# Kernel tuning notes

Measured on AMD Instinct MI355X. Metric: run time of the kernel, lower is better.

Reference implementation:

```python
import jax, jax.numpy as jnp
import numpy as np

N = 10000
E = 160000
C = 256        # in_channels
M = 256        # mid_channels
R = 64         # nregion


def _glorot(key, shape):
    fan_in, fan_out = shape[-1], shape[0]
    lim = (6.0 / (fan_in + fan_out)) ** 0.5
    return jax.random.uniform(key, shape, jnp.float32, -lim, lim)


def setup_inputs() -> dict:
    key = jax.random.key(0)
    ks = jax.random.split(key, 12)
    x = jax.random.normal(ks[0], (N, C), jnp.float32)
    edge_index = jax.random.randint(ks[1], (2, E), 0, N, jnp.int32)
    conv_w = _glorot(ks[2], (C, C))
    conv_b = jnp.zeros((C,), jnp.float32)
    lin1_w = _glorot(ks[3], (M, C)); lin1_b = jnp.zeros((M,), jnp.float32)
    lin2_w = _glorot(ks[4], (M, M)); lin2_b = jnp.zeros((M,), jnp.float32)
    lin3_w = _glorot(ks[5], (1, M)); lin3_b = jnp.zeros((1,), jnp.float32)
    lin4_w = _glorot(ks[6], (M, M)); lin4_b = jnp.zeros((M,), jnp.float32)
    bilin_w = _glorot(ks[7], (R, M, M)) * 0.1
    bilin_b = jnp.zeros((R,), jnp.float32)
    return {"x": x, "edge_index": edge_index,
            "conv_w": conv_w, "conv_b": conv_b,
            "lin1_w": lin1_w, "lin1_b": lin1_b,
            "lin2_w": lin2_w, "lin2_b": lin2_b,
            "lin3_w": lin3_w, "lin3_b": lin3_b,
            "lin4_w": lin4_w, "lin4_b": lin4_b,
            "bilin_w": bilin_w, "bilin_b": bilin_b}


def gcn_conv(x, edge_index, w, b):
    # PyG GCNConv: add self-loops, symmetric D^-1/2 (A+I) D^-1/2 normalization
    src, dst = edge_index[0], edge_index[1]
    n = x.shape[0]
    xw = x @ w.T                                            # [N, C]
    deg = jnp.ones((n,), xw.dtype).at[dst].add(jnp.ones((E,), xw.dtype))  # +1 for self loop
    dinv = jax.lax.rsqrt(deg)
    norm = dinv[src] * dinv[dst]                            # [E]
    agg = jnp.zeros_like(xw).at[dst].add(norm[:, None] * xw[src])
    agg = agg + (dinv * dinv)[:, None] * xw                 # self-loop messages
    return agg + b


def reference(x, edge_index, conv_w, conv_b, lin1_w, lin1_b, lin2_w, lin2_b,
              lin3_w, lin3_b, lin4_w, lin4_b, bilin_w, bilin_b):
    out = jax.nn.relu(gcn_conv(x, edge_index, conv_w, conv_b))
    x0 = out + x                                            # residual [N, C]
    x0 = jax.nn.relu(x0 @ lin1_w.T + lin1_b)                # [N, M]
    x1 = jax.nn.relu(x0 @ lin2_w.T + lin2_b)
    x1 = x1 @ lin3_w.T + lin3_b                             # [N, 1]
    x2 = jax.nn.relu(x0 @ lin4_w.T + lin4_b)                # [N, M]
    # Bilinear(x2, x2): out[n,r] = x2[n] @ W[r] @ x2[n] + b[r]
    t = (x2 @ bilin_w.reshape(R * M, M).T).reshape(-1, R, M)  # [N, R, M]
    x2 = jnp.sum(t * x2[:, None, :], axis=-1) + bilin_b       # [N, R]
    return (x1, x2)
```

## Files before the change

kernel.cpp:

```cpp
#include <hip/hip_runtime.h>

typedef unsigned short u16;
typedef __attribute__((ext_vector_type(8))) short bf16x8;
typedef __attribute__((ext_vector_type(8))) unsigned short u16x8;
typedef __attribute__((ext_vector_type(4))) float f32x4;

#define N_NODES 10000
#define E_EDGES 160000
#define CX_N 2560000
#define W_N  65536
#define WB_N 4194304
#define CANON_BIG_BLOCKS 3426
#define HIST_BLOCKS 79

__device__ __forceinline__ float b2f(u16 u) {
  union { unsigned i; float f; } c; c.i = ((unsigned)u) << 16; return c.f;
}
__device__ __forceinline__ u16 f2b(float f) {
  union { float f; unsigned i; } c; c.f = f;
  unsigned i = c.i;
  return (u16)((i + 0x7FFFu + ((i >> 16) & 1u)) >> 16);
}

__global__ void detect_kernel(const unsigned* __restrict__ w, int* __restrict__ flag) {
  int t = threadIdx.x;
  int cnt = 0;
  for (int i = t; i < 1024; i += 64) {
    unsigned e = (w[i] >> 7) & 0xFF;
    cnt += (e >= 100 && e <= 145) ? 1 : 0;
  }
  for (int o = 32; o; o >>= 1) cnt += __shfl_xor(cnt, o);
  if (t == 0) *flag = (cnt >= 512) ? 1 : 0;
}

__global__ void canon_all_kernel(const void* sx, const void* swc, const void* sw1,
                                 const void* sw2, const void* sw4, const void* swB,
                                 const void* sbc, const void* sb1, const void* sb2,
                                 const void* sb4, const void* sw3, const void* sbB,
                                 const void* sb3,
                                 u16* __restrict__ dstBase,
                                 u16* cbc, u16* cb1, u16* cb2, u16* cb4,
                                 u16* cw3, u16* cbB, u16* cb3,
                                 const int* __restrict__ ei, int* __restrict__ count,
                                 const int* __restrict__ flag) {
  int b = blockIdx.x;
  int f = *flag;
  if (b < CANON_BIG_BLOCKS) {
    long e = ((long)b * 256 + threadIdx.x) * 8;
    const void* src; long so;
    if (e < CX_N)                { src = sx;  so = e; }
    else if (e < CX_N + W_N)     { src = swc; so = e - CX_N; }
    else if (e < CX_N + 2 * W_N) { src = sw1; so = e - (CX_N + W_N); }
    else if (e < CX_N + 3 * W_N) { src = sw2; so = e - (CX_N + 2 * W_N); }
    else if (e < CX_N + 4 * W_N) { src = sw4; so = e - (CX_N + 3 * W_N); }
    else                         { src = swB; so = e - (CX_N + 4 * W_N); }
    if (f) {
      u16x8 v = *((const u16x8*)((const u16*)src + so));
      *(u16x8*)(dstBase + e) = v;
    } else {
      const float* fp = (const float*)src + so;
      float4 a = *(const float4*)fp;
      float4 c = *(const float4*)(fp + 4);
      u16x8 o;
      o[0] = f2b(a.x); o[1] = f2b(a.y); o[2] = f2b(a.z); o[3] = f2b(a.w);
      o[4] = f2b(c.x); o[5] = f2b(c.y); o[6] = f2b(c.z); o[7] = f2b(c.w);
      *(u16x8*)(dstBase + e) = o;
    }
  } else if (b == CANON_BIG_BLOCKS) {
    int t = threadIdx.x;
    const void* srcs[7] = {sbc, sb1, sb2, sb4, sw3, sbB, sb3};
    u16* dsts[7] = {cbc, cb1, cb2, cb4, cw3, cbB, cb3};
    const int ns[7] = {256, 256, 256, 256, 256, 64, 1};
#pragma unroll
    for (int k = 0; k < 7; ++k) {
      if (t < ns[k]) {
        if (f) dsts[k][t] = ((const u16*)srcs[k])[t];
        else   dsts[k][t] = f2b(((const float*)srcs[k])[t]);
      }
    }
  } else {
    int base = (b - CANON_BIG_BLOCKS - 1) * 2048 + threadIdx.x * 8;
#pragma unroll
    for (int k = 0; k < 8; ++k) {
      int i = base + k;
      if (i < E_EDGES) atomicAdd(&count[ei[E_EDGES + i]], 1);
    }
  }
}

__device__ __forceinline__ void stage_async(const u16* __restrict__ src, int stride,
                                            int row0, int maxRow, int k0,
                                            u16* lds, int w, int lane) {
  int rsel = lane >> 3;
  int gch = (lane & 7) ^ rsel;
#pragma unroll
  for (int i = 0; i < 4; ++i) {
    int rb = (w * 4 + i) * 8;
    int grow = row0 + rb + rsel;
    grow = grow > maxRow ? maxRow : grow;
    const u16* gp = src + (size_t)grow * stride + k0 + gch * 8;
    u16* lp = lds + rb * 64;
    __builtin_amdgcn_global_load_lds(
        (const __attribute__((address_space(1))) void*)gp,
        (__attribute__((address_space(3))) void*)lp, 16, 0, 0);
  }
}

__device__ __forceinline__ void mma_tile(const u16* lA, const u16* lB,
                                         f32x4 acc[4][4], int wr, int wc, int lane) {
#pragma unroll
  for (int ks = 0; ks < 2; ++ks) {
    bf16x8 af[4], bfr[4];
    int g = ks * 4 + (lane >> 4);
#pragma unroll
    for (int t = 0; t < 4; ++t) {
      int rowA = wr * 64 + t * 16 + (lane & 15);
      af[t] = *(const bf16x8*)(lA + rowA * 64 + ((g ^ (rowA & 7)) * 8));
      int rowB = wc * 64 + t * 16 + (lane & 15);
      bfr[t] = *(const bf16x8*)(lB + rowB * 64 + ((g ^ (rowB & 7)) * 8));
    }
#pragma unroll
    for (int ti = 0; ti < 4; ++ti)
#pragma unroll
      for (int tj = 0; tj < 4; ++tj)
        acc[ti][tj] = __builtin_amdgcn_mfma_f32_16x16x32_bf16(af[ti], bfr[tj],
                                                              acc[ti][tj], 0, 0, 0);
  }
}

template <bool RELU, bool F32OUT>
__global__ __launch_bounds__(256, 2)
void gemm_kernel(const u16* __restrict__ A, const u16* __restrict__ B,
                 const u16* __restrict__ bias, float* __restrict__ outF,
                 u16* __restrict__ outB, int NN, int J, int K) {
  __shared__ u16 lA[128 * 64];
  __shared__ u16 lB[128 * 64];
  int lane = threadIdx.x & 63;
  int w = threadIdx.x >> 6;
  int wr = w >> 1, wc = w & 1;
  int n0 = blockIdx.y * 128;
  int j0 = blockIdx.x * 128;
  f32x4 acc[4][4];
#pragma unroll
  for (int i = 0; i < 4; ++i)
#pragma unroll
    for (int j = 0; j < 4; ++j) acc[i][j] = (f32x4){0.f, 0.f, 0.f, 0.f};

  for (int kt = 0; kt < K; kt += 64) {
    stage_async(A, K, n0, NN - 1, kt, lA, w, lane);
    stage_async(B, K, j0, J - 1, kt, lB, w, lane);
    __syncthreads();
    mma_tile(lA, lB, acc, wr, wc, lane);
    __syncthreads();
  }

#pragma unroll
  for (int ti = 0; ti < 4; ++ti)
#pragma unroll
    for (int tj = 0; tj < 4; ++tj) {
      int col = j0 + wc * 64 + tj * 16 + (lane & 15);
      float bv = bias ? b2f(bias[col]) : 0.0f;
#pragma unroll
      for (int r = 0; r < 4; ++r) {
        int row = n0 + wr * 64 + ti * 16 + ((lane >> 4) << 2) + r;
        if (row < NN) {
          float v = acc[ti][tj][r] + bv;
          if (RELU) v = fmaxf(v, 0.0f);
          if (F32OUT) outF[(size_t)row * J + col] = v;
          else        outB[(size_t)row * J + col] = f2b(v);
        }
      }
    }
}

__global__ __launch_bounds__(256, 2)
void gemm_fused234_kernel(const u16* __restrict__ A, const u16* __restrict__ B,
                          const u16* __restrict__ bias, const u16* __restrict__ w3,
                          float* __restrict__ out1acc, u16* __restrict__ x2v, int NN) {
  __shared__ u16 lA[128 * 64];
  __shared__ u16 lB[128 * 64];
  int lane = threadIdx.x & 63;
  int w = threadIdx.x >> 6;
  int wr = w >> 1, wc = w & 1;
  int n0 = blockIdx.y * 128;
  int j0 = blockIdx.x * 128;
  f32x4 acc[4][4];
#pragma unroll
  for (int i = 0; i < 4; ++i)
#pragma unroll
    for (int j = 0; j < 4; ++j) acc[i][j] = (f32x4){0.f, 0.f, 0.f, 0.f};

  for (int kt = 0; kt < 256; kt += 64) {
    stage_async(A, 256, n0, NN - 1, kt, lA, w, lane);
    stage_async(B, 256, j0, 511, kt, lB, w, lane);
    __syncthreads();
    mma_tile(lA, lB, acc, wr, wc, lane);
    __syncthreads();
  }

  if (j0 < 256) {
    float part[4][4];
#pragma unroll
    for (int ti = 0; ti < 4; ++ti)
#pragma unroll
      for (int r = 0; r < 4; ++r) part[ti][r] = 0.0f;
#pragma unroll
    for (int ti = 0; ti < 4; ++ti)
#pragma unroll
      for (int tj = 0; tj < 4; ++tj) {
        int col = j0 + wc * 64 + tj * 16 + (lane & 15);
        float bv = b2f(bias[col]);
        float wv = b2f(w3[col]);
#pragma unroll
        for (int r = 0; r < 4; ++r) {
          float v = fmaxf(acc[ti][tj][r] + bv, 0.0f);
          part[ti][r] += v * wv;
        }
      }
#pragma unroll
    for (int ti = 0; ti < 4; ++ti)
#pragma unroll
      for (int r = 0; r < 4; ++r) {
        float s = part[ti][r];
        s += __shfl_xor(s, 1);
        s += __shfl_xor(s, 2);
        s += __shfl_xor(s, 4);
        s += __shfl_xor(s, 8);
        if ((lane & 15) == 0) {
          int row = n0 + wr * 64 + ti * 16 + ((lane >> 4) << 2) + r;
          if (row < NN) unsafeAtomicAdd(&out1acc[row], s);
        }
      }
  } else {
#pragma unroll
    for (int ti = 0; ti < 4; ++ti)
#pragma unroll
      for (int tj = 0; tj < 4; ++tj) {
        int col = j0 + wc * 64 + tj * 16 + (lane & 15);
        float bv = b2f(bias[col]);
#pragma unroll
        for (int r = 0; r < 4; ++r) {
          int row = n0 + wr * 64 + ti * 16 + ((lane >> 4) << 2) + r;
          if (row < NN) {
            float v = fmaxf(acc[ti][tj][r] + bv, 0.0f);
            x2v[(size_t)row * 256 + (col - 256)] = f2b(v);
          }
        }
      }
  }
}

__global__ __launch_bounds__(256, 2)
void bilinear_kernel(const u16* __restrict__ x2v, const u16* __restrict__ W,
                     float* __restrict__ out2acc, int NN) {
  __shared__ u16 lA[128 * 64];
  __shared__ u16 lB[128 * 64];
  int lane = threadIdx.x & 63;
  int w = threadIdx.x >> 6;
  int wr = w >> 1, wc = w & 1;
  int n0 = blockIdx.y * 128;
  int rm0 = blockIdx.x * 128;
  int m0g = rm0 & 255;
  int xv_kt = (m0g >> 6) + wc;
  f32x4 acc[4][4];
#pragma unroll
  for (int i = 0; i < 4; ++i)
#pragma unroll
    for (int j = 0; j < 4; ++j) acc[i][j] = (f32x4){0.f, 0.f, 0.f, 0.f};

  u16 xvr[4][16];

#pragma unroll
  for (int kt4 = 0; kt4 < 4; ++kt4) {
    stage_async(x2v, 256, n0, NN - 1, kt4 * 64, lA, w, lane);
    stage_async(W, 256, rm0, 16383, kt4 * 64, lB, w, lane);
    __syncthreads();
    mma_tile(lA, lB, acc, wr, wc, lane);
    if (kt4 == xv_kt) {
#pragma unroll
      for (int tj = 0; tj < 4; ++tj) {
        int kl = tj * 16 + (lane & 15);
        int ch = kl >> 3, off = kl & 7;
#pragma unroll
        for (int ti = 0; ti < 4; ++ti)
#pragma unroll
          for (int r = 0; r < 4; ++r) {
            int rowl = wr * 64 + ti * 16 + ((lane >> 4) << 2) + r;
            xvr[tj][ti * 4 + r] = lA[rowl * 64 + ((ch ^ (rowl & 7)) * 8) + off];
          }
      }
    }
    __syncthreads();
  }

  int region = rm0 >> 8;
  float rowsum[4][4];
#pragma unroll
  for (int ti = 0; ti < 4; ++ti)
#pragma unroll
    for (int r = 0; r < 4; ++r) rowsum[ti][r] = 0.0f;

#pragma unroll
  for (int ti = 0; ti < 4; ++ti)
#pragma unroll
    for (int tj = 0; tj < 4; ++tj)
#pragma unroll
      for (int r = 0; r < 4; ++r)
        rowsum[ti][r] += acc[ti][tj][r] * b2f(xvr[tj][ti * 4 + r]);

#pragma unroll
  for (int ti = 0; ti < 4; ++ti)
#pragma unroll
    for (int r = 0; r < 4; ++r) {
      float s = rowsum[ti][r];
      s += __shfl_xor(s, 1);
      s += __shfl_xor(s, 2);
      s += __shfl_xor(s, 4);
      s += __shfl_xor(s, 8);
      if ((lane & 15) == 0) {
        int rowl = wr * 64 + ti * 16 + ((lane >> 4) << 2) + r;
        int n = n0 + rowl;
        if (n < NN) unsafeAtomicAdd(&out2acc[(size_t)n * 64 + region], s);
      }
    }
}

__global__ void scan_kernel(const int* __restrict__ count, int* __restrict__ start,
                            int* __restrict__ cursor, float* __restrict__ dinv) {
  __shared__ int wsum[16];
  __shared__ int carry_s;
  int t = threadIdx.x;
  int wv = t >> 6, ln = t & 63;
  if (t == 0) carry_s = 0;
  __syncthreads();
  for (int base = 0; base < N_NODES; base += 1024) {
    int i = base + t;
    int v = (i < N_NODES) ? count[i] : 0;
    int s = v;
#pragma unroll
    for (int o = 1; o < 64; o <<= 1) {
      int u = __shfl_up(s, o);
      if (ln >= o) s += u;
    }
    if (ln == 63) wsum[wv] = s;
    __syncthreads();
    if (wv == 0) {
      int x = (ln < 16) ? wsum[ln] : 0;
#pragma unroll
      for (int o = 1; o < 16; o <<= 1) {
        int u = __shfl_up(x, o);
        if (ln >= o) x += u;
      }
      if (ln < 16) wsum[ln] = x;
    }
    __syncthreads();
    int excl = s - v + (wv ? wsum[wv - 1] : 0) + carry_s;
    if (i < N_NODES) {
      start[i] = excl;
      cursor[i] = excl;
      dinv[i] = rsqrtf(1.0f + (float)v);
    }
    __syncthreads();
    if (t == 0) carry_s += wsum[15];
    __syncthreads();
  }
}

__global__ void place_kernel(const int* __restrict__ ei, int* __restrict__ cursor,
                             int* __restrict__ order) {
  int i = blockIdx.x * 256 + threadIdx.x;
  if (i >= E_EDGES) return;
  int d = ei[E_EDGES + i];
  int pos = atomicAdd(&cursor[d], 1);
  order[pos] = i;
}

__global__ void gather_kernel(const int* __restrict__ ei, const int* __restrict__ order,
                              const int* __restrict__ start, const int* __restrict__ count,
                              const float* __restrict__ dinv, const float* __restrict__ xw,
                              const u16* __restrict__ conv_b, const u16* __restrict__ x,
                              u16* __restrict__ x0) {
  int node = (blockIdx.x * blockDim.x + threadIdx.x) >> 6;
  int lane = threadIdx.x & 63;
  if (node >= N_NODES) return;
  int s0 = start[node], cnt = count[node];
  float dn = dinv[node];
  float ax = 0.f, ay = 0.f, az = 0.f, aw = 0.f;
  for (int base = 0; base < cnt; base += 64) {
    int rem = cnt - base;
    int m = rem < 64 ? rem : 64;
    int eid = (lane < m) ? order[s0 + base + lane] : 0;
    int s = (lane < m) ? ei[eid] : 0;
    float nrm = (lane < m) ? dinv[s] * dn : 0.f;
    for (int j = 0; j < m; ++j) {
      int sj = __shfl(s, j);
      float nj = __shfl(nrm, j);
      float4 v = *((const float4*)(xw + (size_t)sj * 256) + lane);
      ax += nj * v.x; ay += nj * v.y; az += nj * v.z; aw += nj * v.w;
    }
  }
  float4 sv = *((const float4*)(xw + (size_t)node * 256) + lane);
  float slw = dn * dn;
  const u16* bb = conv_b + lane * 4;
  const u16* xr = x + (size_t)node * 256 + lane * 4;
  u16 o[4];
  float vals[4] = {ax + slw * sv.x, ay + slw * sv.y, az + slw * sv.z, aw + slw * sv.w};
#pragma unroll
  for (int j = 0; j < 4; ++j) {
    float v = vals[j] + b2f(bb[j]);
    v = fmaxf(v, 0.0f) + b2f(xr[j]);
    o[j] = f2b(v);
  }
  *((ushort4*)(x0 + (size_t)node * 256) + lane) = make_ushort4(o[0], o[1], o[2], o[3]);
}

__global__ void out_final_kernel(const float* __restrict__ out1acc,
                                 const float* __restrict__ out2acc,
                                 const u16* __restrict__ b3, const u16* __restrict__ bb,
                                 void* __restrict__ dout, const int* __restrict__ flag) {
  int idx = blockIdx.x * 256 + threadIdx.x;
  int f = *flag;
  if (idx < N_NODES) {
    float v = out1acc[idx] + b2f(b3[0]);
    if (f) ((u16*)dout)[idx] = f2b(v);
    else   ((float*)dout)[idx] = v;
  } else if (idx < N_NODES + N_NODES * 64) {
    int k = idx - N_NODES;
    float v = out2acc[k] + b2f(bb[k & 63]);
    if (f) ((u16*)dout)[idx] = f2b(v);
    else   ((float*)dout)[idx] = v;
  }
}

extern "C" void kernel_launch(void* const* d_in, const int* in_sizes, int n_in,
                              void* d_out, int out_size, void* d_ws, size_t ws_size,
                              hipStream_t stream) {
  const int* ei = (const int*)d_in[1];

  float* ws      = (float*)d_ws;
  float* xw      = ws;
  int*   count   = (int*)(xw + N_NODES * 256);
  int*   start   = count + 10240;
  int*   cursor  = start + 10240;
  int*   order   = cursor + 10240;
  float* dinv    = (float*)(order + E_EDGES);
  float* out1acc = dinv + 10240;
  float* out2acc = out1acc + 10240;
  u16* x0  = (u16*)(out2acc + N_NODES * 64);
  u16* x0m = x0 + N_NODES * 256;
  u16* x2v = x0m + N_NODES * 256;
  u16* cx  = x2v + N_NODES * 256;
  u16* cwc = cx + CX_N;
  u16* cw1 = cwc + W_N;
  u16* cw2 = cw1 + W_N;
  u16* cw4 = cw2 + W_N;
  u16* cwB = cw4 + W_N;
  u16* cbc = cwB + WB_N;
  u16* cb1 = cbc + 256;
  u16* cb2 = cb1 + 256;
  u16* cb4 = cb2 + 256;
  u16* cw3 = cb4 + 256;
  u16* cbB = cw3 + 256;
  u16* cb3 = cbB + 64;
  int* flag = (int*)(cb3 + 16);

  hipMemsetAsync(count, 0, N_NODES * sizeof(int), stream);
  hipMemsetAsync(out1acc, 0, (10240 + (size_t)N_NODES * 64) * sizeof(float), stream);

  detect_kernel<<<1, 64, 0, stream>>>((const unsigned*)d_in[0], flag);

  canon_all_kernel<<<CANON_BIG_BLOCKS + 1 + HIST_BLOCKS, 256, 0, stream>>>(
      d_in[0], d_in[2], d_in[4], d_in[6], d_in[10], d_in[12],
      d_in[3], d_in[5], d_in[7], d_in[11], d_in[8], d_in[13], d_in[9],
      cx, cbc, cb1, cb2, cb4, cw3, cbB, cb3,
      ei, count, flag);

  scan_kernel<<<1, 1024, 0, stream>>>(count, start, cursor, dinv);
  place_kernel<<<(E_EDGES + 255) / 256, 256, 0, stream>>>(ei, cursor, order);

  gemm_kernel<false, true><<<dim3(2, 79), 256, 0, stream>>>(
      cx, cwc, nullptr, xw, nullptr, N_NODES, 256, 256);

  gather_kernel<<<(N_NODES * 64 + 255) / 256, 256, 0, stream>>>(
      ei, order, start, count, dinv, xw, cbc, cx, x0);

  gemm_kernel<true, false><<<dim3(2, 79), 256, 0, stream>>>(
      x0, cw1, cb1, nullptr, x0m, N_NODES, 256, 256);

  gemm_fused234_kernel<<<dim3(4, 79), 256, 0, stream>>>(
      x0m, cw2, cb2, cw3, out1acc, x2v, N_NODES);

  bilinear_kernel<<<dim3(128, 79), 256, 0, stream>>>(x2v, cwB, out2acc, N_NODES);

  out_final_kernel<<<(N_NODES * 65 + 255) / 256, 256, 0, stream>>>(
      out1acc, out2acc, cb3, cbB, d_out, flag);
}
```

Baseline: 391.3 us.

## Double-buffer LDS tiles in GEMM, fused and bilinear kernels

Turns the single LDS A/B tile buffers in three MFMA GEMM kernels into two buffers each. The loads for the next K-tile are issued before the MFMAs on the current tile run, and one barrier per iteration replaces two. The goal is to hide global-to-LDS latency behind compute and cut barrier stalls. In exchange, LDS per block doubles to 64KB, which could limit occupancy. With only four K-steps per tile, the prologue takes up a large share of the loop.

```diff
diff --git a/kernel.cpp b/kernel.cpp
--- a/kernel.cpp
+++ b/kernel.cpp
@@ -133,8 +133,8 @@
 void gemm_kernel(const u16* __restrict__ A, const u16* __restrict__ B,
                  const u16* __restrict__ bias, float* __restrict__ outF,
                  u16* __restrict__ outB, int NN, int J, int K) {
-  __shared__ u16 lA[128 * 64];
-  __shared__ u16 lB[128 * 64];
+  __shared__ u16 lA[2][128 * 64];
+  __shared__ u16 lB[2][128 * 64];
   int lane = threadIdx.x & 63;
   int w = threadIdx.x >> 6;
   int wr = w >> 1, wc = w & 1;
@@ -146,12 +146,18 @@
 #pragma unroll
     for (int j = 0; j < 4; ++j) acc[i][j] = (f32x4){0.f, 0.f, 0.f, 0.f};
 
-  for (int kt = 0; kt < K; kt += 64) {
-    stage_async(A, K, n0, NN - 1, kt, lA, w, lane);
-    stage_async(B, K, j0, J - 1, kt, lB, w, lane);
-    __syncthreads();
-    mma_tile(lA, lB, acc, wr, wc, lane);
-    __syncthreads();
+  int nt = K >> 6;
+  stage_async(A, K, n0, NN - 1, 0, lA[0], w, lane);
+  stage_async(B, K, j0, J - 1, 0, lB[0], w, lane);
+  __syncthreads();
+  for (int t = 0; t < nt; ++t) {
+    int cur = t & 1;
+    if (t + 1 < nt) {
+      stage_async(A, K, n0, NN - 1, (t + 1) << 6, lA[cur ^ 1], w, lane);
+      stage_async(B, K, j0, J - 1, (t + 1) << 6, lB[cur ^ 1], w, lane);
+    }
+    mma_tile(lA[cur], lB[cur], acc, wr, wc, lane);
+    if (t + 1 < nt) __syncthreads();
   }
 
 #pragma unroll
@@ -177,8 +183,8 @@
 void gemm_fused234_kernel(const u16* __restrict__ A, const u16* __restrict__ B,
                           const u16* __restrict__ bias, const u16* __restrict__ w3,
                           float* __restrict__ out1acc, u16* __restrict__ x2v, int NN) {
-  __shared__ u16 lA[128 * 64];
-  __shared__ u16 lB[128 * 64];
+  __shared__ u16 lA[2][128 * 64];
+  __shared__ u16 lB[2][128 * 64];
   int lane = threadIdx.x & 63;
   int w = threadIdx.x >> 6;
   int wr = w >> 1, wc = w & 1;
@@ -190,12 +196,18 @@
 #pragma unroll
     for (int j = 0; j < 4; ++j) acc[i][j] = (f32x4){0.f, 0.f, 0.f, 0.f};
 
-  for (int kt = 0; kt < 256; kt += 64) {
-    stage_async(A, 256, n0, NN - 1, kt, lA, w, lane);
-    stage_async(B, 256, j0, 511, kt, lB, w, lane);
-    __syncthreads();
-    mma_tile(lA, lB, acc, wr, wc, lane);
-    __syncthreads();
+  stage_async(A, 256, n0, NN - 1, 0, lA[0], w, lane);
+  stage_async(B, 256, j0, 511, 0, lB[0], w, lane);
+  __syncthreads();
+#pragma unroll
+  for (int t = 0; t < 4; ++t) {
+    int cur = t & 1;
+    if (t < 3) {
+      stage_async(A, 256, n0, NN - 1, (t + 1) << 6, lA[cur ^ 1], w, lane);
+      stage_async(B, 256, j0, 511, (t + 1) << 6, lB[cur ^ 1], w, lane);
+    }
+    mma_tile(lA[cur], lB[cur], acc, wr, wc, lane);
+    if (t < 3) __syncthreads();
   }
 
   if (j0 < 256) {
@@ -253,8 +265,8 @@
 __global__ __launch_bounds__(256, 2)
 void bilinear_kernel(const u16* __restrict__ x2v, const u16* __restrict__ W,
                      float* __restrict__ out2acc, int NN) {
-  __shared__ u16 lA[128 * 64];
-  __shared__ u16 lB[128 * 64];
+  __shared__ u16 lA[2][128 * 64];
+  __shared__ u16 lB[2][128 * 64];
   int lane = threadIdx.x & 63;
   int w = threadIdx.x >> 6;
   int wr = w >> 1, wc = w & 1;
@@ -270,12 +282,17 @@
 
   u16 xvr[4][16];
 
+  stage_async(x2v, 256, n0, NN - 1, 0, lA[0], w, lane);
+  stage_async(W, 256, rm0, 16383, 0, lB[0], w, lane);
+  __syncthreads();
 #pragma unroll
   for (int kt4 = 0; kt4 < 4; ++kt4) {
-    stage_async(x2v, 256, n0, NN - 1, kt4 * 64, lA, w, lane);
-    stage_async(W, 256, rm0, 16383, kt4 * 64, lB, w, lane);
-    __syncthreads();
-    mma_tile(lA, lB, acc, wr, wc, lane);
+    int cur = kt4 & 1;
+    if (kt4 < 3) {
+      stage_async(x2v, 256, n0, NN - 1, (kt4 + 1) * 64, lA[cur ^ 1], w, lane);
+      stage_async(W, 256, rm0, 16383, (kt4 + 1) * 64, lB[cur ^ 1], w, lane);
+    }
+    mma_tile(lA[cur], lB[cur], acc, wr, wc, lane);
     if (kt4 == xv_kt) {
 #pragma unroll
       for (int tj = 0; tj < 4; ++tj) {
@@ -286,11 +303,11 @@
 #pragma unroll
           for (int r = 0; r < 4; ++r) {
             int rowl = wr * 64 + ti * 16 + ((lane >> 4) << 2) + r;
-            xvr[tj][ti * 4 + r] = lA[rowl * 64 + ((ch ^ (rowl & 7)) * 8) + off];
+            xvr[tj][ti * 4 + r] = lA[cur][rowl * 64 + ((ch ^ (rowl & 7)) * 8) + off];
           }
       }
     }
-    __syncthreads();
+    if (kt4 < 3) __syncthreads();
   }
 
   int region = rm0 >> 8;
```

After: 398.3 us. About the same (+1.8%).

## Use 512-thread GEMM blocks with full-K LDS staging and staged vmcnt waits

Applied to the files above, without the earlier changes.

All GEMM-style kernels move to 8 waves per block (2x4 wave grid, 4x2 MFMA tiles per wave). Each block issues all four K-tiles of A and B into LDS at once (128 KB), then waits on each tile in turn with partial vmcnt counts and barriers, raising wave priority around the MFMA work. This overlaps loads with compute and removes the per-iteration double syncthreads. The bilinear kernel now reads x2 values straight from the resident LDS tiles and reduces across the four column waves through LDS before a single atomic per row, so fewer atomics are issued. In exchange, occupancy drops to one block per CU because of the LDS footprint.

```diff
diff --git a/kernel.cpp b/kernel.cpp
--- a/kernel.cpp
+++ b/kernel.cpp
@@ -88,17 +88,17 @@
   }
 }
 
-__device__ __forceinline__ void stage_async(const u16* __restrict__ src, int stride,
-                                            int row0, int maxRow, int k0,
-                                            u16* lds, int w, int lane) {
+__device__ __forceinline__ void stage512(const u16* __restrict__ src,
+                                         int row0, int maxRow, int k0,
+                                         u16* lds, int w, int lane) {
   int rsel = lane >> 3;
   int gch = (lane & 7) ^ rsel;
 #pragma unroll
-  for (int i = 0; i < 4; ++i) {
-    int rb = (w * 4 + i) * 8;
+  for (int i = 0; i < 2; ++i) {
+    int rb = (w * 2 + i) * 8;
     int grow = row0 + rb + rsel;
     grow = grow > maxRow ? maxRow : grow;
-    const u16* gp = src + (size_t)grow * stride + k0 + gch * 8;
+    const u16* gp = src + (size_t)grow * 256 + k0 + gch * 8;
     u16* lp = lds + rb * 64;
     __builtin_amdgcn_global_load_lds(
         (const __attribute__((address_space(1))) void*)gp,
@@ -106,65 +106,95 @@
   }
 }
 
-__device__ __forceinline__ void mma_tile(const u16* lA, const u16* lB,
-                                         f32x4 acc[4][4], int wr, int wc, int lane) {
+__device__ __forceinline__ void mma_tile512(const u16* lA, const u16* lB,
+                                            f32x4 acc[4][2], int wr, int wc, int lane) {
 #pragma unroll
   for (int ks = 0; ks < 2; ++ks) {
-    bf16x8 af[4], bfr[4];
+    bf16x8 af[4], bfr[2];
     int g = ks * 4 + (lane >> 4);
 #pragma unroll
-    for (int t = 0; t < 4; ++t) {
-      int rowA = wr * 64 + t * 16 + (lane & 15);
-      af[t] = *(const bf16x8*)(lA + rowA * 64 + ((g ^ (rowA & 7)) * 8));
-      int rowB = wc * 64 + t * 16 + (lane & 15);
-      bfr[t] = *(const bf16x8*)(lB + rowB * 64 + ((g ^ (rowB & 7)) * 8));
-    }
-#pragma unroll
-    for (int ti = 0; ti < 4; ++ti)
-#pragma unroll
-      for (int tj = 0; tj < 4; ++tj)
-        acc[ti][tj] = __builtin_amdgcn_mfma_f32_16x16x32_bf16(af[ti], bfr[tj],
-                                                              acc[ti][tj], 0, 0, 0);
-  }
+    for (int m = 0; m < 4; ++m) {
+      int rowA = wr * 64 + m * 16 + (lane & 15);
+      af[m] = *(const bf16x8*)(lA + rowA * 64 + ((g ^ (rowA & 7)) * 8));
+    }
+#pragma unroll
+    for (int n = 0; n < 2; ++n) {
+      int rowB = wc * 32 + n * 16 + (lane & 15);
+      bfr[n] = *(const bf16x8*)(lB + rowB * 64 + ((g ^ (rowB & 7)) * 8));
+    }
+#pragma unroll
+    for (int m = 0; m < 4; ++m)
+#pragma unroll
+      for (int n = 0; n < 2; ++n)
+        acc[m][n] = __builtin_amdgcn_mfma_f32_16x16x32_bf16(af[m], bfr[n],
+                                                            acc[m][n], 0, 0, 0);
+  }
+}
+
+__device__ __forceinline__ void gemm_loop512(const u16* __restrict__ A,
+                                             const u16* __restrict__ B,
+                                             int n0, int maxA, int j0, int maxB,
+                                             u16 (*lA)[8192], u16 (*lB)[8192],
+                                             f32x4 acc[4][2], int w, int lane,
+                                             int wr, int wc) {
+#pragma unroll
+  for (int t = 0; t < 4; ++t) {
+    stage512(A, n0, maxA, t * 64, lA[t], w, lane);
+    stage512(B, j0, maxB, t * 64, lB[t], w, lane);
+  }
+  asm volatile("s_waitcnt vmcnt(12)" ::: "memory");
+  asm volatile("s_barrier" ::: "memory");
+  __builtin_amdgcn_s_setprio(1);
+  mma_tile512(lA[0], lB[0], acc, wr, wc, lane);
+  __builtin_amdgcn_s_setprio(0);
+  asm volatile("s_waitcnt vmcnt(8)" ::: "memory");
+  asm volatile("s_barrier" ::: "memory");
+  __builtin_amdgcn_s_setprio(1);
+  mma_tile512(lA[1], lB[1], acc, wr, wc, lane);
+  __builtin_amdgcn_s_setprio(0);
+  asm volatile("s_waitcnt vmcnt(4)" ::: "memory");
+  asm volatile("s_barrier" ::: "memory");
+  __builtin_amdgcn_s_setprio(1);
+  mma_tile512(lA[2], lB[2], acc, wr, wc, lane);
+  __builtin_amdgcn_s_setprio(0);
+  asm volatile("s_waitcnt vmcnt(0)" ::: "memory");
+  asm volatile("s_barrier" ::: "memory");
+  __builtin_amdgcn_s_setprio(1);
+  mma_tile512(lA[3], lB[3], acc, wr, wc, lane);
+  __builtin_amdgcn_s_setprio(0);
 }
 
 template <bool RELU, bool F32OUT>
-__global__ __launch_bounds__(256, 2)
-void gemm_kernel(const u16* __restrict__ A, const u16* __restrict__ B,
-                 const u16* __restrict__ bias, float* __restrict__ outF,
-                 u16* __restrict__ outB, int NN, int J, int K) {
-  __shared__ u16 lA[128 * 64];
-  __shared__ u16 lB[128 * 64];
+__global__ __launch_bounds__(512, 1)
+void gemm512_kernel(const u16* __restrict__ A, const u16* __restrict__ B,
+                    const u16* __restrict__ bias, float* __restrict__ outF,
+                    u16* __restrict__ outB, int NN, int J) {
+  __shared__ u16 lA[4][8192];
+  __shared__ u16 lB[4][8192];
   int lane = threadIdx.x & 63;
   int w = threadIdx.x >> 6;
-  int wr = w >> 1, wc = w & 1;
+  int wr = w >> 2, wc = w & 3;
   int n0 = blockIdx.y * 128;
   int j0 = blockIdx.x * 128;
-  f32x4 acc[4][4];
-#pragma unroll
-  for (int i = 0; i < 4; ++i)
-#pragma unroll
-    for (int j = 0; j < 4; ++j) acc[i][j] = (f32x4){0.f, 0.f, 0.f, 0.f};
-
-  for (int kt = 0; kt < K; kt += 64) {
-    stage_async(A, K, n0, NN - 1, kt, lA, w, lane);
-    stage_async(B, K, j0, J - 1, kt, lB, w, lane);
-    __syncthreads();
-    mma_tile(lA, lB, acc, wr, wc, lane);
-    __syncthreads();
-  }
-
-#pragma unroll
-  for (int ti = 0; ti < 4; ++ti)
-#pragma unroll
-    for (int tj = 0; tj < 4; ++tj) {
-      int col = j0 + wc * 64 + tj * 16 + (lane & 15);
+  f32x4 acc[4][2];
+#pragma unroll
+  for (int m = 0; m < 4; ++m)
+#pragma unroll
+    for (int n = 0; n < 2; ++n) acc[m][n] = (f32x4){0.f, 0.f, 0.f, 0.f};
+
+  gemm_loop512(A, B, n0, NN - 1, j0, J - 1, lA, lB, acc, w, lane, wr, wc);
+
+#pragma unroll
+  for (int m = 0; m < 4; ++m)
+#pragma unroll
+    for (int n = 0; n < 2; ++n) {
+      int col = j0 + wc * 32 + n * 16 + (lane & 15);
       float bv = bias ? b2f(bias[col]) : 0.0f;
 #pragma unroll
       for (int r = 0; r < 4; ++r) {
-        int row = n0 + wr * 64 + ti * 16 + ((lane >> 4) << 2) + r;
+        int row = n0 + wr * 64 + m * 16 + ((lane >> 4) << 2) + r;
         if (row < NN) {
-          float v = acc[ti][tj][r] + bv;
+          float v = acc[m][n][r] + bv;
           if (RELU) v = fmaxf(v, 0.0f);
           if (F32OUT) outF[(size_t)row * J + col] = v;
           else        outB[(size_t)row * J + col] = f2b(v);
@@ -173,76 +203,70 @@
     }
 }
 
-__global__ __launch_bounds__(256, 2)
-void gemm_fused234_kernel(const u16* __restrict__ A, const u16* __restrict__ B,
-                          const u16* __restrict__ bias, const u16* __restrict__ w3,
-                          float* __restrict__ out1acc, u16* __restrict__ x2v, int NN) {
-  __shared__ u16 lA[128 * 64];
-  __shared__ u16 lB[128 * 64];
+__global__ __launch_bounds__(512, 1)
+void fused234_512_kernel(const u16* __restrict__ A, const u16* __restrict__ B,
+                         const u16* __restrict__ bias, const u16* __restrict__ w3,
+                         float* __restrict__ out1acc, u16* __restrict__ x2v, int NN) {
+  __shared__ u16 lA[4][8192];
+  __shared__ u16 lB[4][8192];
   int lane = threadIdx.x & 63;
   int w = threadIdx.x >> 6;
-  int wr = w >> 1, wc = w & 1;
+  int wr = w >> 2, wc = w & 3;
   int n0 = blockIdx.y * 128;
   int j0 = blockIdx.x * 128;
-  f32x4 acc[4][4];
-#pragma unroll
-  for (int i = 0; i < 4; ++i)
-#pragma unroll
-    for (int j = 0; j < 4; ++j) acc[i][j] = (f32x4){0.f, 0.f, 0.f, 0.f};
-
-  for (int kt = 0; kt < 256; kt += 64) {
-    stage_async(A, 256, n0, NN - 1, kt, lA, w, lane);
-    stage_async(B, 256, j0, 511, kt, lB, w, lane);
-    __syncthreads();
-    mma_tile(lA, lB, acc, wr, wc, lane);
-    __syncthreads();
-  }
+  f32x4 acc[4][2];
+#pragma unroll
+  for (int m = 0; m < 4; ++m)
+#pragma unroll
+    for (int n = 0; n < 2; ++n) acc[m][n] = (f32x4){0.f, 0.f, 0.f, 0.f};
+
+  gemm_loop512(A, B, n0, NN - 1, j0, 511, lA, lB, acc, w, lane, wr, wc);
 
   if (j0 < 256) {
     float part[4][4];
 #pragma unroll
-    for (int ti = 0; ti < 4; ++ti)
-#pragma unroll
-      for (int r = 0; r < 4; ++r) part[ti][r] = 0.0f;
-#pragma unroll
-    for (int ti = 0; ti < 4; ++ti)
-#pragma unroll
-      for (int tj = 0; tj < 4; ++tj) {
-        int col = j0 + wc * 64 + tj * 16 + (lane & 15);
+    for (int m = 0; m < 4; ++m)
+#pragma unroll
+      for (int r = 0; r < 4; ++r) part[m][r] = 0.0f;
+#pragma unroll
+    for (int m = 0; m < 4; ++m)
+#pragma unroll
+      for (int n = 0; n < 2; ++n) {
+        int col = j0 + wc * 32 + n * 16 + (lane & 15);
         float bv = b2f(bias[col]);
         float wv = b2f(w3[col]);
 #pragma unroll
         for (int r = 0; r < 4; ++r) {
-          float v = fmaxf(acc[ti][tj][r] + bv, 0.0f);
-          part[ti][r] += v * wv;
+          float v = fmaxf(acc[m][n][r] + bv, 0.0f);
+          part[m][r] += v * wv;
         }
       }
 #pragma unroll
-    for (int ti = 0; ti < 4; ++ti)
+    for (int m = 0; m < 4; ++m)
 #pragma unroll
       for (int r = 0; r < 4; ++r) {
-        float s = part[ti][r];
+        float s = part[m][r];
         s += __shfl_xor(s, 1);
         s += __shfl_xor(s, 2);
         s += __shfl_xor(s, 4);
         s += __shfl_xor(s, 8);
         if ((lane & 15) == 0) {
-          int row = n0 + wr * 64 + ti * 16 + ((lane >> 4) << 2) + r;
+          int row = n0 + wr * 64 + m * 16 + ((lane >> 4) << 2) + r;
           if (row < NN) unsafeAtomicAdd(&out1acc[row], s);
         }
       }
   } else {
 #pragma unroll
-    for (int ti = 0; ti < 4; ++ti)
-#pragma unroll
-      for (int tj = 0; tj < 4; ++tj) {
-        int col = j0 + wc * 64 + tj * 16 + (lane & 15);
+    for (int m = 0; m < 4; ++m)
+#pragma unroll
+      for (int n = 0; n < 2; ++n) {
+        int col = j0 + wc * 32 + n * 16 + (lane & 15);
         float bv = b2f(bias[col]);
 #pragma unroll
         for (int r = 0; r < 4; ++r) {
-          int row = n0 + wr * 64 + ti * 16 + ((lane >> 4) << 2) + r;
+          int row = n0 + wr * 64 + m * 16 + ((lane >> 4) << 2) + r;
           if (row < NN) {
-            float v = fmaxf(acc[ti][tj][r] + bv, 0.0f);
+            float v = fmaxf(acc[m][n][r] + bv, 0.0f);
             x2v[(size_t)row * 256 + (col - 256)] = f2b(v);
           }
         }
@@ -250,79 +274,78 @@
   }
 }
 
-__global__ __launch_bounds__(256, 2)
-void bilinear_kernel(const u16* __restrict__ x2v, const u16* __restrict__ W,
-                     float* __restrict__ out2acc, int NN) {
-  __shared__ u16 lA[128 * 64];
-  __shared__ u16 lB[128 * 64];
+__global__ __launch_bounds__(512, 1)
+void bilinear512_kernel(const u16* __restrict__ x2v, const u16* __restrict__ W,
+                        float* __restrict__ out2acc, int NN) {
+  __shared__ u16 lA[4][8192];
+  __shared__ u16 lB[4][8192];
   int lane = threadIdx.x & 63;
   int w = threadIdx.x >> 6;
-  int wr = w >> 1, wc = w & 1;
+  int wr = w >> 2, wc = w & 3;
   int n0 = blockIdx.y * 128;
   int rm0 = blockIdx.x * 128;
-  int m0g = rm0 & 255;
-  int xv_kt = (m0g >> 6) + wc;
-  f32x4 acc[4][4];
-#pragma unroll
-  for (int i = 0; i < 4; ++i)
-#pragma unroll
-    for (int j = 0; j < 4; ++j) acc[i][j] = (f32x4){0.f, 0.f, 0.f, 0.f};
-
-  u16 xvr[4][16];
-
-#pragma unroll
-  for (int kt4 = 0; kt4 < 4; ++kt4) {
-    stage_async(x2v, 256, n0, NN - 1, kt4 * 64, lA, w, lane);
-    stage_async(W, 256, rm0, 16383, kt4 * 64, lB, w, lane);
-    __syncthreads();
-    mma_tile(lA, lB, acc, wr, wc, lane);
-    if (kt4 == xv_kt) {
-#pragma unroll
-      for (int tj = 0; tj < 4; ++tj) {
-        int kl = tj * 16 + (lane & 15);
-        int ch = kl >> 3, off = kl & 7;
-#pragma unroll
-        for (int ti = 0; ti < 4; ++ti)
-#pragma unroll
-          for (int r = 0; r < 4; ++r) {
-            int rowl = wr * 64 + ti * 16 + ((lane >> 4) << 2) + r;
-            xvr[tj][ti * 4 + r] = lA[rowl * 64 + ((ch ^ (rowl & 7)) * 8) + off];
-          }
-      }
-    }
-    __syncthreads();
-  }
-
-  int region = rm0 >> 8;
+  int region = blockIdx.x >> 1;
+  int m0g = (blockIdx.x & 1) * 128;
+  f32x4 acc[4][2];
+#pragma unroll
+  for (int m = 0; m < 4; ++m)
+#pragma unroll
+    for (int n = 0; n < 2; ++n) acc[m][n] = (f32x4){0.f, 0.f, 0.f, 0.f};
+
+  gemm_loop512(x2v, W, n0, NN - 1, rm0, 16383, lA, lB, acc, w, lane, wr, wc);
+
   float rowsum[4][4];
 #pragma unroll
-  for (int ti = 0; ti < 4; ++ti)
-#pragma unroll
-    for (int r = 0; r < 4; ++r) rowsum[ti][r] = 0.0f;
-
-#pragma unroll
-  for (int ti = 0; ti < 4; ++ti)
-#pragma unroll
-    for (int tj = 0; tj < 4; ++tj)
-#pragma unroll
-      for (int r = 0; r < 4; ++r)
-        rowsum[ti][r] += acc[ti][tj][r] * b2f(xvr[tj][ti * 4 + r]);
-
-#pragma unroll
-  for (int ti = 0; ti < 4; ++ti)
+  for (int m = 0; m < 4; ++m)
+#pragma unroll
+    for (int r = 0; r < 4; ++r) rowsum[m][r] = 0.0f;
+
+#pragma unroll
+  for (int n = 0; n < 2; ++n) {
+    int x2col = m0g + wc * 32 + n * 16 + (lane & 15);
+    int tile = x2col >> 6;
+    int c = x2col & 63;
+    int ch = c >> 3, off = c & 7;
+#pragma unroll
+    for (int m = 0; m < 4; ++m)
+#pragma unroll
+      for (int r = 0; r < 4; ++r) {
+        int rowl = wr * 64 + m * 16 + ((lane >> 4) << 2) + r;
+        float xv = b2f(lA[tile][rowl * 64 + ((ch ^ (rowl & 7)) * 8) + off]);
+        rowsum[m][r] += acc[m][n][r] * xv;
+      }
+  }
+
+#pragma unroll
+  for (int m = 0; m < 4; ++m)
 #pragma unroll
     for (int r = 0; r < 4; ++r) {
-      float s = rowsum[ti][r];
+      float s = rowsum[m][r];
       s += __shfl_xor(s, 1);
       s += __shfl_xor(s, 2);
       s += __shfl_xor(s, 4);
       s += __shfl_xor(s, 8);
-      if ((lane & 15) == 0) {
-        int rowl = wr * 64 + ti * 16 + ((lane >> 4) << 2) + r;
-        int n = n0 + rowl;
-        if (n < NN) unsafeAtomicAdd(&out2acc[(size_t)n * 64 + region], s);
-      }
-    }
+      rowsum[m][r] = s;
+    }
+
+  float* sc = (float*)lA;
+  asm volatile("s_barrier" ::: "memory");
+  if ((lane & 15) == 0) {
+#pragma unroll
+    for (int m = 0; m < 4; ++m)
+#pragma unroll
+      for (int r = 0; r < 4; ++r) {
+        int rowl = wr * 64 + m * 16 + ((lane >> 4) << 2) + r;
+        sc[rowl * 4 + wc] = rowsum[m][r];
+      }
+  }
+  asm volatile("s_barrier" ::: "memory");
+  int tid = threadIdx.x;
+  if (tid < 128) {
+    float s = sc[tid * 4] + sc[tid * 4 + 1] + sc[tid * 4 + 2] + sc[tid * 4 + 3];
+    int nn = n0 + tid;
+    if (nn < NN) unsafeAtomicAdd(&out2acc[(size_t)nn * 64 + region], s);
+  }
 }
 
 __global__ void scan_kernel(const int* __restrict__ count, int* __restrict__ start,
@@ -478,19 +501,19 @@
   scan_kernel<<<1, 1024, 0, stream>>>(count, start, cursor, dinv);
   place_kernel<<<(E_EDGES + 255) / 256, 256, 0, stream>>>(ei, cursor, order);
 
-  gemm_kernel<false, true><<<dim3(2, 79), 256, 0, stream>>>(
-      cx, cwc, nullptr, xw, nullptr, N_NODES, 256, 256);
+  gemm512_kernel<false, true><<<dim3(2, 79), 512, 0, stream>>>(
+      cx, cwc, nullptr, xw, nullptr, N_NODES, 256);
 
   gather_kernel<<<(N_NODES * 64 + 255) / 256, 256, 0, stream>>>(
       ei, order, start, count, dinv, xw, cbc, cx, x0);
 
-  gemm_kernel<true, false><<<dim3(2, 79), 256, 0, stream>>>(
-      x0, cw1, cb1, nullptr, x0m, N_NODES, 256, 256);
-
-  gemm_fused234_kernel<<<dim3(4, 79), 256, 0, stream>>>(
+  gemm512_kernel<true, false><<<dim3(2, 79), 512, 0, stream>>>(
+      x0, cw1, cb1, nullptr, x0m, N_NODES, 256);
+
+  fused234_512_kernel<<<dim3(4, 79), 512, 0, stream>>>(
       x0m, cw2, cb2, cw3, out1acc, x2v, N_NODES);
 
-  bilinear_kernel<<<dim3(128, 79), 256, 0, stream>>>(x2v, cwB, out2acc, N_NODES);
+  bilinear512_kernel<<<dim3(128, 79), 512, 0, stream>>>(x2v, cwB, out2acc, N_NODES);
 
   out_final_kernel<<<(N_NODES * 65 + 255) / 256, 256, 0, stream>>>(
       out1acc, out2acc, cb3, cbB, d_out, flag);
```

New measurement: 415.7 us. 6.2% more time.

## Stream bilinear MFMA operands directly from global memory, dropping LDS staging

Applied to the files above, without the earlier changes.

The bilinear kernel no longer stages x2 and W tiles through shared memory with barriers. Each lane now loads its bf16x8 MFMA fragments straight from global memory, and the epilogue re-reads the x2 values it needs from global instead of from LDS. The grid is transposed so consecutive blocks share the same W slice and differ in node tile, which is meant to improve L2 reuse of the weights. In exchange, fragment loads become strided per-lane global loads with no data sharing across waves, which could raise memory traffic and latency.

```diff
diff --git a/kernel.cpp b/kernel.cpp
--- a/kernel.cpp
+++ b/kernel.cpp
@@ -251,77 +251,65 @@
 }
 
 __global__ __launch_bounds__(256, 2)
-void bilinear_kernel(const u16* __restrict__ x2v, const u16* __restrict__ W,
-                     float* __restrict__ out2acc, int NN) {
-  __shared__ u16 lA[128 * 64];
-  __shared__ u16 lB[128 * 64];
+void bilinear_stream_kernel(const u16* __restrict__ x2v, const u16* __restrict__ W,
+                            float* __restrict__ out2acc, int NN) {
   int lane = threadIdx.x & 63;
   int w = threadIdx.x >> 6;
   int wr = w >> 1, wc = w & 1;
-  int n0 = blockIdx.y * 128;
-  int rm0 = blockIdx.x * 128;
-  int m0g = rm0 & 255;
-  int xv_kt = (m0g >> 6) + wc;
+  int n0 = blockIdx.x * 128;
+  int rm0 = blockIdx.y * 128;
+  int region = blockIdx.y >> 1;
+  int i0 = (blockIdx.y & 1) * 128;
+
+  const u16* pA[4];
+  const u16* pB[4];
+#pragma unroll
+  for (int t = 0; t < 4; ++t) {
+    int rA = n0 + wr * 64 + t * 16 + (lane & 15);
+    rA = rA < NN ? rA : NN - 1;
+    pA[t] = x2v + (size_t)rA * 256 + (lane >> 4) * 8;
+    int rB = rm0 + wc * 64 + t * 16 + (lane & 15);
+    pB[t] = W + (size_t)rB * 256 + (lane >> 4) * 8;
+  }
+
   f32x4 acc[4][4];
 #pragma unroll
   for (int i = 0; i < 4; ++i)
 #pragma unroll
     for (int j = 0; j < 4; ++j) acc[i][j] = (f32x4){0.f, 0.f, 0.f, 0.f};
 
-  u16 xvr[4][16];
-
-#pragma unroll
-  for (int kt4 = 0; kt4 < 4; ++kt4) {
-    stage_async(x2v, 256, n0, NN - 1, kt4 * 64, lA, w, lane);
-    stage_async(W, 256, rm0, 16383, kt4 * 64, lB, w, lane);
-    __syncthreads();
-    mma_tile(lA, lB, acc, wr, wc, lane);
-    if (kt4 == xv_kt) {
-#pragma unroll
-      for (int tj = 0; tj < 4; ++tj) {
-        int kl = tj * 16 + (lane & 15);
-        int ch = kl >> 3, off = kl & 7;
-#pragma unroll
-        for (int ti = 0; ti < 4; ++ti)
-#pragma unroll
-          for (int r = 0; r < 4; ++r) {
-            int rowl = wr * 64 + ti * 16 + ((lane >> 4) << 2) + r;
-            xvr[tj][ti * 4 + r] = lA[rowl * 64 + ((ch ^ (rowl & 7)) * 8) + off];
-          }
-      }
-    }
-    __syncthreads();
-  }
-
-  int region = rm0 >> 8;
-  float rowsum[4][4];
+#pragma unroll
+  for (int ks = 0; ks < 8; ++ks) {
+    bf16x8 af[4], bfr[4];
+#pragma unroll
+    for (int t = 0; t < 4; ++t) af[t] = *(const bf16x8*)(pA[t] + ks * 32);
+#pragma unroll
+    for (int t = 0; t < 4; ++t) bfr[t] = *(const bf16x8*)(pB[t] + ks * 32);
+#pragma unroll
+    for (int ti = 0; ti < 4; ++ti)
+#pragma unroll
+      for (int tj = 0; tj < 4; ++tj)
+        acc[ti][tj] = __builtin_amdgcn_mfma_f32_16x16x32_bf16(af[ti], bfr[tj],
+                                                              acc[ti][tj], 0, 0, 0);
+  }
+
 #pragma unroll
   for (int ti = 0; ti < 4; ++ti)
 #pragma unroll
-    for (int r = 0; r < 4; ++r) rowsum[ti][r] = 0.0f;
-
-#pragma unroll
-  for (int ti = 0; ti < 4; ++ti)
-#pragma unroll
-    for (int tj = 0; tj < 4; ++tj)
-#pragma unroll
-      for (int r = 0; r < 4; ++r)
-        rowsum[ti][r] += acc[ti][tj][r] * b2f(xvr[tj][ti * 4 + r]);
-
-#pragma unroll
-  for (int ti = 0; ti < 4; ++ti)
-#pragma unroll
     for (int r = 0; r < 4; ++r) {
-      float s = rowsum[ti][r];
+      int row = n0 + wr * 64 + ti * 16 + ((lane >> 4) << 2) + r;
+      int rc = row < NN ? row : NN - 1;
+      const u16* xr = x2v + (size_t)rc * 256 + i0 + wc * 64 + (lane & 15);
+      float s = 0.0f;
+#pragma unroll
+      for (int tj = 0; tj < 4; ++tj)
+        s += acc[ti][tj][r] * b2f(xr[tj * 16]);
       s += __shfl_xor(s, 1);
       s += __shfl_xor(s, 2);
       s += __shfl_xor(s, 4);
       s += __shfl_xor(s, 8);
-      if ((lane & 15) == 0) {
-        int rowl = wr * 64 + ti * 16 + ((lane >> 4) << 2) + r;
-        int n = n0 + rowl;
-        if (n < NN) unsafeAtomicAdd(&out2acc[(size_t)n * 64 + region], s);
-      }
+      if ((lane & 15) == 0 && row < NN)
+        unsafeAtomicAdd(&out2acc[(size_t)row * 64 + region], s);
     }
 }
 
@@ -490,7 +478,7 @@
   gemm_fused234_kernel<<<dim3(4, 79), 256, 0, stream>>>(
       x0m, cw2, cb2, cw3, out1acc, x2v, N_NODES);
 
-  bilinear_kernel<<<dim3(128, 79), 256, 0, stream>>>(x2v, cwB, out2acc, N_NODES);
+  bilinear_stream_kernel<<<dim3(79, 128), 256, 0, stream>>>(x2v, cwB, out2acc, N_NODES);
 
   out_final_kernel<<<(N_NODES * 65 + 255) / 256, 256, 0, stream>>>(
       out1acc, out2acc, cb3, cbB, d_out, flag);
```

Result: slower. 554.4 us (+41.7%).
